# Kernel tuning notes

Measured on AMD Instinct MI355X. Metric: run time of the kernel, lower is better.

The kernel has to match this reference:

```python
import jax, jax.numpy as jnp
import numpy as np

FEAT_STRIDE = 16
PRE_NMS_TOP_N = 4000   # cfg[cfg_key].RPN_PRE_NMS_TOP_N
POST_NMS_TOP_N = 300   # cfg[cfg_key].RPN_POST_NMS_TOP_N
NMS_THRESH = 0.7       # cfg[cfg_key].RPN_NMS_THRESH


def _generate_anchors(base_size=16, ratios=(0.5, 1.0, 2.0), scales=(8, 16, 32)):
    ratios = np.array(ratios, dtype=np.float64)
    scales = np.array(scales, dtype=np.float64)
    base = np.array([1, 1, base_size, base_size], dtype=np.float64) - 1

    def whctrs(a):
        w = a[2] - a[0] + 1
        h = a[3] - a[1] + 1
        return w, h, a[0] + 0.5 * (w - 1), a[1] + 0.5 * (h - 1)

    def mk(ws, hs, xc, yc):
        ws = np.atleast_1d(ws)[:, None]
        hs = np.atleast_1d(hs)[:, None]
        return np.hstack((xc - 0.5 * (ws - 1), yc - 0.5 * (hs - 1),
                          xc + 0.5 * (ws - 1), yc + 0.5 * (hs - 1)))

    w, h, xc, yc = whctrs(base)
    size = w * h
    ws = np.round(np.sqrt(size / ratios))
    hs = np.round(ws * ratios)
    ratio_anchors = mk(ws, hs, xc, yc)
    out = []
    for i in range(ratio_anchors.shape[0]):
        w, h, xc, yc = whctrs(ratio_anchors[i])
        out.append(mk(w * scales, h * scales, xc, yc))
    return np.vstack(out).astype(np.float32)  # [9,4]


def _nms_keep(boxes, thresh):
    # boxes sorted by score desc, [N,4]; torchvision-style IoU (no +1).
    x1, y1, x2, y2 = boxes[:, 0], boxes[:, 1], boxes[:, 2], boxes[:, 3]
    areas = (x2 - x1) * (y2 - y1)
    lt = jnp.maximum(boxes[:, None, :2], boxes[None, :, :2])
    rb = jnp.minimum(boxes[:, None, 2:], boxes[None, :, 2:])
    wh = jnp.clip(rb - lt, 0.0)
    inter = wh[..., 0] * wh[..., 1]
    iou = inter / (areas[:, None] + areas[None, :] - inter + 1e-9)  # [N,N]
    N = boxes.shape[0]
    idx = jnp.arange(N)
    def body(i, keep):
        sup = (iou[i] > thresh) & (idx > i) & keep[i]
        return keep & ~sup
    return jax.lax.fori_loop(0, N, body, jnp.ones((N,), jnp.bool_))


def _per_image(boxes, scores):
    # pre-NMS top-k by score (matches sort-desc + slice)
    _, order = jax.lax.top_k(scores, PRE_NMS_TOP_N)
    b = boxes[order]
    keep = _nms_keep(jax.lax.stop_gradient(b), NMS_THRESH)
    rank = jnp.cumsum(keep) - 1                       # position among kept
    tgt = jnp.where(keep, rank, POST_NMS_TOP_N)       # OOB indices are dropped
    return jnp.zeros((POST_NMS_TOP_N, 4), boxes.dtype).at[tgt].set(b, mode='drop')


def reference(scores, bbox_deltas, im_info, anchors):
    B, A, H, W = scores.shape
    # anchor shifts over the feature grid
    sx = jnp.arange(W, dtype=scores.dtype) * FEAT_STRIDE
    sy = jnp.arange(H, dtype=scores.dtype) * FEAT_STRIDE
    yy, xx = jnp.meshgrid(sy, sx, indexing='ij')
    shifts = jnp.stack([xx.ravel(), yy.ravel(), xx.ravel(), yy.ravel()], axis=1)  # [K,4]
    all_anchors = (anchors[None, :, :] + shifts[:, None, :]).reshape(-1, 4)       # [K*A,4]

    deltas = bbox_deltas.transpose(0, 2, 3, 1).reshape(B, -1, 4)  # [B,K*A,4]
    sc = scores.transpose(0, 2, 3, 1).reshape(B, -1)              # [B,K*A]

    # bbox_transform_inv
    w = all_anchors[:, 2] - all_anchors[:, 0] + 1.0
    h = all_anchors[:, 3] - all_anchors[:, 1] + 1.0
    cx = all_anchors[:, 0] + 0.5 * w
    cy = all_anchors[:, 1] + 0.5 * h
    pcx = deltas[..., 0] * w + cx
    pcy = deltas[..., 1] * h + cy
    pw = jnp.exp(deltas[..., 2]) * w
    ph = jnp.exp(deltas[..., 3]) * h
    props = jnp.stack([pcx - 0.5 * pw, pcy - 0.5 * ph,
                       pcx + 0.5 * pw, pcy + 0.5 * ph], axis=-1)  # [B,K*A,4]

    # clip_boxes: x in [0, im_w-1], y in [0, im_h-1]
    hi = jnp.stack([im_info[:, 1] - 1, im_info[:, 0] - 1,
                    im_info[:, 1] - 1, im_info[:, 0] - 1], axis=1)  # [B,4]
    props = jnp.clip(props, 0.0, hi[:, None, :])

    boxes_out = jax.vmap(_per_image)(props, sc)  # [B,POST,4]
    batch_col = jnp.broadcast_to(
        jnp.arange(B, dtype=scores.dtype)[:, None, None], (B, POST_NMS_TOP_N, 1))
    return jnp.concatenate([batch_col, boxes_out], axis=-1)  # [B,POST,5]


def setup_inputs():
    key = jax.random.key(0)
    k1, k2 = jax.random.split(key)
    B, A, H, W = 4, 9, 50, 76
    scores = jax.random.normal(k1, (B, A, H, W), jnp.float32)
    bbox_deltas = jax.random.normal(k2, (B, 4 * A, H, W), jnp.float32) * 0.2
    im_info = jnp.tile(jnp.array([[800.0, 1216.0, 1.0]], jnp.float32), (B, 1))
    anchors = jnp.asarray(_generate_anchors())
    return {"scores": scores, "bbox_deltas": bbox_deltas,
            "im_info": im_info, "anchors": anchors}
```

## Files before the change

kernel.cpp:

```cpp
#include <hip/hip_runtime.h>
#include <stdint.h>

#define A_N 9
#define H_N 50
#define W_N 76
#define HW_N (H_N * W_N)
#define N_PROP (A_N * HW_N)
#define B_N 4
#define PRE_NMS 4000
#define POST_NMS 300
#define NMS_TH 0.7f
#define SORT_N 4096
#define MASK_WORDS 64
#define CAND_MAX 5120
#define NBINS 4096
#define NPAIR 32
#define NLW 5
#define NDELTA 6
#define DEC_BLKS ((N_PROP + 255) / 256)

__global__ __launch_bounds__(256) void decode_kernel(
    const float* __restrict__ scores,
    const float* __restrict__ deltas,
    const float* __restrict__ im_info,
    const float* __restrict__ anchors,
    float4* __restrict__ boxes,
    unsigned long long* __restrict__ keys) {
#pragma clang fp contract(off)
    int tid = threadIdx.x;
    int b = blockIdx.y;
    int r = blockIdx.x * 256 + tid;
    if (r >= N_PROP) return;

    int a = r / HW_N;
    int hw = r - a * HW_N;
    int hy = hw / W_N;
    int wx = hw - hy * W_N;

    float sx = (float)wx * 16.0f;
    float sy = (float)hy * 16.0f;
    float ax1 = anchors[a * 4 + 0] + sx;
    float ay1 = anchors[a * 4 + 1] + sy;
    float ax2 = anchors[a * 4 + 2] + sx;
    float ay2 = anchors[a * 4 + 3] + sy;
    float aw = ax2 - ax1 + 1.0f;
    float ah = ay2 - ay1 + 1.0f;
    float cx = ax1 + 0.5f * aw;
    float cy = ay1 + 0.5f * ah;

    const float* db = deltas + ((size_t)b * 36 + (size_t)a * 4) * HW_N + hw;
    float d0 = db[0];
    float d1 = db[HW_N];
    float d2 = db[2 * HW_N];
    float d3 = db[3 * HW_N];

    float pcx = d0 * aw + cx;
    float pcy = d1 * ah + cy;
    float pw  = expf(d2) * aw;
    float ph  = expf(d3) * ah;

    float x1 = pcx - 0.5f * pw;
    float y1 = pcy - 0.5f * ph;
    float x2 = pcx + 0.5f * pw;
    float y2 = pcy + 0.5f * ph;

    float xhi = im_info[b * 3 + 1] - 1.0f;
    float yhi = im_info[b * 3 + 0] - 1.0f;
    x1 = fminf(fmaxf(x1, 0.0f), xhi);
    y1 = fminf(fmaxf(y1, 0.0f), yhi);
    x2 = fminf(fmaxf(x2, 0.0f), xhi);
    y2 = fminf(fmaxf(y2, 0.0f), yhi);

    boxes[(size_t)b * N_PROP + r] = make_float4(x1, y1, x2, y2);

    float s = scores[((size_t)b * A_N + a) * HW_N + hw];
    unsigned f = __float_as_uint(s);
    unsigned sk = f ^ ((f & 0x80000000u) ? 0xFFFFFFFFu : 0x80000000u);
    unsigned n_ref = (unsigned)(hw * A_N + a);
    unsigned long long key = ((unsigned long long)sk << 32) | (unsigned)(~n_ref);
    keys[(size_t)b * N_PROP + r] = key;
}

__global__ __launch_bounds__(1024) void mid_kernel(
    const unsigned long long* __restrict__ keys,
    unsigned* __restrict__ cnt,
    unsigned long long* __restrict__ cand) {
    __shared__ unsigned hist[NBINS];
    __shared__ int Tlds;
    __shared__ unsigned cntL;
    const int b = blockIdx.x;
    const int tid = threadIdx.x;

    for (int i = tid; i < NBINS; i += 1024) hist[i] = 0u;
    if (tid == 0) cntL = 0u;
    __syncthreads();

    for (int it = 0; it < (N_PROP + 1023) / 1024; ++it) {
        int n = it * 1024 + tid;
        if (n < N_PROP) {
            unsigned long long k = keys[(size_t)b * N_PROP + n];
            atomicAdd(&hist[(unsigned)(k >> 52)], 1u);
        }
    }
    __syncthreads();

    if (tid < 64) {
        int lane = tid;
        unsigned gsum = 0;
        for (int j = 0; j < 64; ++j) gsum += hist[lane * 64 + j];
        unsigned s = gsum;
        for (int d = 1; d < 64; d <<= 1) {
            unsigned t = (unsigned)__shfl_down((int)s, d);
            if (lane + d < 64) s += t;
        }
        unsigned long long bal = __ballot(s >= PRE_NMS);
        int gstar = 63 - __builtin_clzll(bal);
        unsigned after = (gstar < 63)
            ? (unsigned)__builtin_amdgcn_readlane((int)s, gstar + 1) : 0u;
        unsigned R = PRE_NMS - after;
        unsigned s2 = hist[gstar * 64 + lane];
        for (int d = 1; d < 64; d <<= 1) {
            unsigned t = (unsigned)__shfl_down((int)s2, d);
            if (lane + d < 64) s2 += t;
        }
        unsigned long long bal2 = __ballot(s2 >= R);
        int j = 63 - __builtin_clzll(bal2);
        if (lane == 0) Tlds = gstar * 64 + j;
    }
    __syncthreads();

    const int Tb = Tlds;
    for (int it = 0; it < (N_PROP + 1023) / 1024; ++it) {
        int n = it * 1024 + tid;
        bool pred = false;
        unsigned long long k = 0ull;
        if (n < N_PROP) {
            k = keys[(size_t)b * N_PROP + n];
            pred = ((int)(unsigned)(k >> 52) >= Tb);
        }
        unsigned long long m = __ballot(pred);
        if (m) {
            int lane = tid & 63;
            int lead = __ffsll((unsigned long long)m) - 1;
            unsigned base = 0;
            if (lane == lead) base = atomicAdd(&cntL, (unsigned)__popcll(m));
            base = __shfl((int)base, lead);
            if (pred) {
                unsigned pos = base + (unsigned)__popcll(m & ((1ull << lane) - 1ull));
                if (pos < CAND_MAX) cand[(size_t)b * CAND_MAX + pos] = k;
            }
        }
    }
    __syncthreads();
    if (tid == 0) cnt[b] = cntL;
}

__global__ __launch_bounds__(256) void rank_scatter_kernel(
    const unsigned long long* __restrict__ cand,
    const unsigned* __restrict__ cnt,
    const float4* __restrict__ boxes,
    float4* __restrict__ sortedBoxes) {
    __shared__ unsigned long long sk[256];
    int b = blockIdx.y;
    int tid = threadIdx.x;
    int ci = blockIdx.x * 64 + (tid >> 2);
    int q = tid & 3;
    int mc = (int)min(cnt[b], (unsigned)CAND_MAX);
    unsigned long long my = (ci < mc) ? cand[(size_t)b * CAND_MAX + ci] : 0ull;
    int rank = 0;
    int nt = (mc + 255) >> 8;
    for (int t = 0; t < nt; ++t) {
        int j = t * 256 + tid;
        sk[tid] = (j < mc) ? cand[(size_t)b * CAND_MAX + j] : 0ull;
        __syncthreads();
#pragma unroll 16
        for (int c = 0; c < 64; ++c) {
            int cc = q * 64 + ((c + q * 17) & 63);
            rank += (sk[cc] > my) ? 1 : 0;
        }
        __syncthreads();
    }
    rank += __shfl_xor(rank, 1);
    rank += __shfl_xor(rank, 2);
    if (q == 0 && ci < mc && rank < PRE_NMS) {
        unsigned n_ref = ~(unsigned)(my & 0xFFFFFFFFull);
        unsigned a = n_ref % A_N;
        unsigned hw = n_ref / A_N;
        sortedBoxes[(size_t)b * SORT_N + rank] =
            boxes[(size_t)b * N_PROP + a * HW_N + hw];
    }
    if (q == 1) {
        int pi = blockIdx.x * 64 + (tid >> 2);
        if (pi >= PRE_NMS && pi < SORT_N)
            sortedBoxes[(size_t)b * SORT_N + pi] = make_float4(0.f, 0.f, 0.f, 0.f);
    }
}

__global__ __launch_bounds__(256) void iou_mask_kernel(
    const float4* __restrict__ sortedBoxes,
    unsigned long long* __restrict__ colmaj,
    unsigned long long* __restrict__ rowmaj,
    unsigned long long* __restrict__ trans) {
#pragma clang fp contract(off)
    int b = blockIdx.y;
    int wv = threadIdx.x >> 6;
    int t = threadIdx.x & 63;
    int k = blockIdx.x * 4 + wv;
    int rc = 0;
    while (k >= 64 - rc) { k -= 64 - rc; ++rc; }
    int cc = rc + k;

    __shared__ float4 colb[4][64];
    colb[wv][t] = sortedBoxes[(size_t)b * SORT_N + cc * 64 + t];
    __syncthreads();

    int r = rc * 64 + t;
    float4 rb = sortedBoxes[(size_t)b * SORT_N + r];
    float rarea = (rb.z - rb.x) * (rb.w - rb.y);
    unsigned long long word = 0ull;
    for (int c = 0; c < 64; ++c) {
        int j = cc * 64 + c;
        float4 cb = colb[wv][c];
        float carea = (cb.z - cb.x) * (cb.w - cb.y);
        float ltx = fmaxf(rb.x, cb.x);
        float lty = fmaxf(rb.y, cb.y);
        float rbx = fminf(rb.z, cb.z);
        float rby = fminf(rb.w, cb.w);
        float iw = fmaxf(rbx - ltx, 0.0f);
        float ih = fmaxf(rby - lty, 0.0f);
        float inter = iw * ih;
        float iou = inter / (rarea + carea - inter + 1e-9f);
        if (iou > NMS_TH && j > r) word |= (1ull << c);
    }
    colmaj[((size_t)b * MASK_WORDS + cc) * SORT_N + r] = word;
    rowmaj[((size_t)b * SORT_N + r) * MASK_WORDS + cc] = word;

    int delta = cc - rc;
    if (delta < NDELTA) {
        unsigned long long tw = 0ull;
        for (int j = 0; j < 64; ++j) {
            unsigned long long bal = __ballot(((word >> j) & 1ull) != 0ull);
            if (t == j) tw = bal;
        }
        trans[(((size_t)b * MASK_WORDS + rc) * NDELTA + delta) * 64 + t] = tw;
    }
}

__device__ __forceinline__ unsigned long long bal_nz(unsigned long long tileT,
                                                     unsigned long long alive) {
    return __ballot((tileT & alive) != 0ull);
}

__device__ __forceinline__ void block_sync() {
    asm volatile("s_waitcnt lgkmcnt(0)" ::: "memory");
    __builtin_amdgcn_s_barrier();
    asm volatile("" ::: "memory");
}

#define GLOAD(dst, addr) \
    asm volatile("global_load_dwordx2 %0, %1, off" : "=v"(dst) : "v"(addr))
#define WAITV0 asm volatile("s_waitcnt vmcnt(0)" ::: "memory")
#define SCHED0 __builtin_amdgcn_sched_barrier(0)

#define TRG(P, t)  ((t) < 6 ? 2 * (P) : 2 * (P) + 1)
#define TRD(P, t)  ((t) < 6 ? (t) : (t) - 6)
#define TRVAL(P, t) (TRG(P, t) + TRD(P, t) < 64)
#define TR_ADDR(P, t) \
    (TR + (((size_t)TRG(P, t) * NDELTA + (TRVAL(P, t) ? TRD(P, t) : 0)) << 6) + lane)

#define ISSUE_PAIR(P)                                                          \
    do {                                                                       \
        pf_vmask = 0u;                                                         \
        GLOAD(pf0,  TR_ADDR(P, 0));  if (TRVAL(P, 0))  pf_vmask |= 1u << 0;    \
        GLOAD(pf1,  TR_ADDR(P, 1));  if (TRVAL(P, 1))  pf_vmask |= 1u << 1;    \
        GLOAD(pf2,  TR_ADDR(P, 2));  if (TRVAL(P, 2))  pf_vmask |= 1u << 2;    \
        GLOAD(pf3,  TR_ADDR(P, 3));  if (TRVAL(P, 3))  pf_vmask |= 1u << 3;    \
        GLOAD(pf4,  TR_ADDR(P, 4));  if (TRVAL(P, 4))  pf_vmask |= 1u << 4;    \
        GLOAD(pf5,  TR_ADDR(P, 5));  if (TRVAL(P, 5))  pf_vmask |= 1u << 5;    \
        GLOAD(pf6,  TR_ADDR(P, 6));  if (TRVAL(P, 6))  pf_vmask |= 1u << 6;    \
        GLOAD(pf7,  TR_ADDR(P, 7));  if (TRVAL(P, 7))  pf_vmask |= 1u << 7;    \
        GLOAD(pf8,  TR_ADDR(P, 8));  if (TRVAL(P, 8))  pf_vmask |= 1u << 8;    \
        GLOAD(pf9,  TR_ADDR(P, 9));  if (TRVAL(P, 9))  pf_vmask |= 1u << 9;    \
        GLOAD(pf10, TR_ADDR(P, 10)); if (TRVAL(P, 10)) pf_vmask |= 1u << 10;   \
    } while (0)

#define NEXTROW2(rk)                                                           \
    int rk;                                                                    \
    {                                                                          \
        if (xA) { int bb_ = __builtin_ctzll(xA); xA &= xA - 1; rk = baseA + bb_; } \
        else if (xB) { int bb_ = __builtin_ctzll(xB); xB &= xB - 1; rk = baseB + bb_; } \
        else rk = rpad;                                                        \
    }

__global__ __launch_bounds__(512, 1) void nms_scan_kernel(
    const unsigned long long* __restrict__ trans,
    const unsigned long long* __restrict__ rowmaj,
    const float4* __restrict__ sortedBoxes,
    float* __restrict__ out) {
    int b = blockIdx.x;
    int tid = threadIdx.x;
    int lane = tid & 63;
    int wv = tid >> 6;
    const unsigned long long* TR = trans + (size_t)b * MASK_WORDS * NDELTA * 64;
    const unsigned long long* R = rowmaj + (size_t)b * SORT_N * MASK_WORDS;

    __shared__ int kept[POST_NMS];
    __shared__ unsigned remW[MASK_WORDS][2];
    __shared__ unsigned long long aliveLds[MASK_WORDS];
    __shared__ unsigned long long ring[4][11][64];
    __shared__ unsigned long long car2[2][2];
    __shared__ int doneLds;
    __shared__ int kcntLds;

    if (tid < MASK_WORDS) { remW[tid][0] = 0u; remW[tid][1] = 0u; aliveLds[tid] = 0ull; }
    if (tid < 4) car2[tid >> 1][tid & 1] = 0ull;
    if (tid == 0) { doneLds = 0; kcntLds = 0; }

    unsigned long long pf0=0,pf1=0,pf2=0,pf3=0,pf4=0,pf5=0,pf6=0,pf7=0,pf8=0,pf9=0,pf10=0;
    unsigned pf_vmask = 0u;
    bool pf_have = false;
    unsigned long long gp0=0,gp1=0,gp2=0,gp3=0,gp4=0,gp5=0,gp6=0,gp7=0;
    bool ld_valid = false;

    if (wv == 1) {
        for (int t = 0; t < 11; ++t) {
            unsigned long long v = TRVAL(0, t)
                ? TR[(((size_t)TRG(0, t)) * NDELTA + TRD(0, t)) * 64 + lane] : 0ull;
            ring[0][t][lane] = v;
        }
        ISSUE_PAIR(1);
        pf_have = true;
    }
    block_sync();

    unsigned long long carA = 0ull, carB = 0ull;
    int kcnt = 0;

    for (int q = 0; q < NPAIR; ++q) {
        if (wv == 0) {
            int A = 2 * q, Bg = A + 1, slot = q & 3;
            unsigned long long dA  = ring[slot][0][lane];
            unsigned long long tA1 = ring[slot][1][lane];
            unsigned long long tA2 = ring[slot][2][lane];
            unsigned long long tA3 = ring[slot][3][lane];
            unsigned long long dB  = ring[slot][6][lane];
            unsigned long long tB1 = ring[slot][7][lane];
            unsigned long long tB2 = ring[slot][8][lane];
            unsigned long long remA =
                ((unsigned long long)remW[A][1] << 32) | (unsigned long long)remW[A][0];
            unsigned long long remB =
                ((unsigned long long)remW[Bg][1] << 32) | (unsigned long long)remW[Bg][0];
            unsigned long long h2A = car2[q & 1][0];
            unsigned long long h2B = car2[q & 1][1];
            bool hit = false;
            unsigned long long aliveA = 0ull, aliveB = 0ull;
            unsigned long long pend = ~(remA | carA | h2A);
            while (pend) {
                int bit = __builtin_ctzll(pend);
                if (lane == 0) kept[kcnt] = (A << 6) + bit;
                ++kcnt;
                aliveA |= 1ull << bit;
                if (kcnt == POST_NMS) { hit = true; break; }
                unsigned long long d = __ballot(((dA >> bit) & 1ull) != 0ull);
                pend &= ~(d | (1ull << bit));
            }
            if (!hit) {
                unsigned long long nA1 = bal_nz(tA1, aliveA);
                pend = ~(remB | carB | h2B | nA1);
                while (pend) {
                    int bit = __builtin_ctzll(pend);
                    if (lane == 0) kept[kcnt] = (Bg << 6) + bit;
                    ++kcnt;
                    aliveB |= 1ull << bit;
                    if (kcnt == POST_NMS) { hit = true; break; }
                    unsigned long long d = __ballot(((dB >> bit) & 1ull) != 0ull);
                    pend &= ~(d | (1ull << bit));
                }
            }
            carA = bal_nz(tA2, aliveA) | bal_nz(tB1, aliveB);
            carB = bal_nz(tA3, aliveA) | bal_nz(tB2, aliveB);
            if (lane == 0) {
                aliveLds[A]  = aliveA;
                aliveLds[Bg] = aliveB;
                kcntLds = kcnt;
                if (hit) doneLds = 1;
            }
        } else if (wv == 1) {
            if (pf_have) {
                WAITV0;
                SCHED0;
                int wp = q + 1;
                if (wp < NPAIR) {
                    int ws = wp & 3;
                    ring[ws][0][lane]  = (pf_vmask & (1u << 0))  ? pf0  : 0ull;
                    ring[ws][1][lane]  = (pf_vmask & (1u << 1))  ? pf1  : 0ull;
                    ring[ws][2][lane]  = (pf_vmask & (1u << 2))  ? pf2  : 0ull;
                    ring[ws][3][lane]  = (pf_vmask & (1u << 3))  ? pf3  : 0ull;
                    ring[ws][4][lane]  = (pf_vmask & (1u << 4))  ? pf4  : 0ull;
                    ring[ws][5][lane]  = (pf_vmask & (1u << 5))  ? pf5  : 0ull;
                    ring[ws][6][lane]  = (pf_vmask & (1u << 6))  ? pf6  : 0ull;
                    ring[ws][7][lane]  = (pf_vmask & (1u << 7))  ? pf7  : 0ull;
                    ring[ws][8][lane]  = (pf_vmask & (1u << 8))  ? pf8  : 0ull;
                    ring[ws][9][lane]  = (pf_vmask & (1u << 9))  ? pf9  : 0ull;
                    ring[ws][10][lane] = (pf_vmask & (1u << 10)) ? pf10 : 0ull;
                }
                pf_have = false;
            }
            int ip = q + 2;
            if (ip < NPAIR) {
                ISSUE_PAIR(ip);
                pf_have = true;
            }
        } else if (wv == 2) {
            if (q >= 1) {
                int p = q - 1, sp = p & 3;
                unsigned long long aA = aliveLds[2 * p];
                unsigned long long aB = aliveLds[2 * p + 1];
                unsigned long long tA4 = ring[sp][4][lane];
                unsigned long long tA5 = ring[sp][5][lane];
                unsigned long long tB3 = ring[sp][9][lane];
                unsigned long long tB4 = ring[sp][10][lane];
                unsigned long long c0 = bal_nz(tA4, aA) | bal_nz(tB3, aB);
                unsigned long long c1 = bal_nz(tA5, aA) | bal_nz(tB4, aB);
                if (lane == 0) {
                    car2[(q + 1) & 1][0] = c0;
                    car2[(q + 1) & 1][1] = c1;
                }
            }
        } else {
            if (ld_valid) {
                WAITV0;
                SCHED0;
                unsigned long long acc =
                    ((gp0 | gp1) | (gp2 | gp3)) | ((gp4 | gp5) | (gp6 | gp7));
                unsigned lo = (unsigned)acc, hi = (unsigned)(acc >> 32);
                if (lo) atomicOr(&remW[lane][0], lo);
                if (hi) atomicOr(&remW[lane][1], hi);
                ld_valid = false;
            }
            if (q >= 1) {
                int p = q - 1, gA = 2 * p, gB = 2 * p + 1;
                unsigned long long aA = aliveLds[gA];
                unsigned long long aB = aliveLds[gB];
                int k = wv - 3;
                unsigned long long below = (1ull << lane) - 1ull;
                bool inA = (aA >> lane) & 1ull;
                bool inB = (aB >> lane) & 1ull;
                int posA = (int)__popcll(aA & below);
                int posB = (int)__popcll(aA) + (int)__popcll(aB & below);
                unsigned long long mA = __ballot(inA && (posA % NLW) == k);
                unsigned long long mB = __ballot(inB && (posB % NLW) == k);
                if (mA | mB) {
                    int baseA = gA << 6, baseB = gB << 6;
                    unsigned long long xA = mA, xB = mB;
                    int rpad = mA ? (baseA + __builtin_ctzll(mA))
                                  : (baseB + __builtin_ctzll(mB));
                    NEXTROW2(r0) NEXTROW2(r1) NEXTROW2(r2) NEXTROW2(r3)
                    NEXTROW2(r4) NEXTROW2(r5) NEXTROW2(r6) NEXTROW2(r7)
                    const unsigned long long* Rb = R + lane;
                    GLOAD(gp0, Rb + (size_t)r0 * MASK_WORDS);
                    GLOAD(gp1, Rb + (size_t)r1 * MASK_WORDS);
                    GLOAD(gp2, Rb + (size_t)r2 * MASK_WORDS);
                    GLOAD(gp3, Rb + (size_t)r3 * MASK_WORDS);
                    GLOAD(gp4, Rb + (size_t)r4 * MASK_WORDS);
                    GLOAD(gp5, Rb + (size_t)r5 * MASK_WORDS);
                    GLOAD(gp6, Rb + (size_t)r6 * MASK_WORDS);
                    GLOAD(gp7, Rb + (size_t)r7 * MASK_WORDS);
                    ld_valid = true;
                    unsigned long long ovf = 0ull;
                    while (xA) {
                        int bb = __builtin_ctzll(xA); xA &= xA - 1;
                        ovf |= Rb[(size_t)(baseA + bb) * MASK_WORDS];
                    }
                    while (xB) {
                        int bb = __builtin_ctzll(xB); xB &= xB - 1;
                        ovf |= Rb[(size_t)(baseB + bb) * MASK_WORDS];
                    }
                    if (ovf) {
                        unsigned lo = (unsigned)ovf, hi = (unsigned)(ovf >> 32);
                        if (lo) atomicOr(&remW[lane][0], lo);
                        if (hi) atomicOr(&remW[lane][1], hi);
                    }
                }
            }
        }
        block_sync();
        if (doneLds) break;
    }

    WAITV0;
    __syncthreads();

    int kc = kcntLds;
    for (int r = tid; r < POST_NMS; r += 512) {
        float* o = out + ((size_t)b * POST_NMS + r) * 5;
        float4 bx = make_float4(0.f, 0.f, 0.f, 0.f);
        if (r < kc) bx = sortedBoxes[(size_t)b * SORT_N + kept[r]];
        o[0] = (float)b;
        o[1] = bx.x;
        o[2] = bx.y;
        o[3] = bx.z;
        o[4] = bx.w;
    }
}

extern "C" void kernel_launch(void* const* d_in, const int* in_sizes, int n_in,
                              void* d_out, int out_size, void* d_ws, size_t ws_size,
                              hipStream_t stream) {
    const float* scores  = (const float*)d_in[0];
    const float* deltas  = (const float*)d_in[1];
    const float* im_info = (const float*)d_in[2];
    const float* anchors = (const float*)d_in[3];
    float* out = (float*)d_out;

    char* ws = (char*)d_ws;
    size_t off = 0;
    float4* boxes = (float4*)(ws + off);
    off += (size_t)B_N * N_PROP * sizeof(float4);
    off = (off + 255) & ~(size_t)255;
    unsigned long long* keys = (unsigned long long*)(ws + off);
    off += (size_t)B_N * N_PROP * sizeof(unsigned long long);
    off = (off + 255) & ~(size_t)255;
    float4* sortedBoxes = (float4*)(ws + off);
    off += (size_t)B_N * SORT_N * sizeof(float4);
    off = (off + 255) & ~(size_t)255;
    unsigned long long* colmaj = (unsigned long long*)(ws + off);
    off += (size_t)B_N * MASK_WORDS * SORT_N * sizeof(unsigned long long);
    off = (off + 255) & ~(size_t)255;
    unsigned long long* rowmaj = (unsigned long long*)(ws + off);
    off += (size_t)B_N * SORT_N * MASK_WORDS * sizeof(unsigned long long);
    off = (off + 255) & ~(size_t)255;
    unsigned long long* trans = (unsigned long long*)(ws + off);
    off += (size_t)B_N * MASK_WORDS * NDELTA * 64 * sizeof(unsigned long long);
    off = (off + 255) & ~(size_t)255;
    unsigned long long* cand = (unsigned long long*)(ws + off);
    off += (size_t)B_N * CAND_MAX * sizeof(unsigned long long);
    off = (off + 255) & ~(size_t)255;
    unsigned* cnt = (unsigned*)(ws + off);
    off += (size_t)B_N * sizeof(unsigned);

    decode_kernel<<<dim3(DEC_BLKS, B_N), 256, 0, stream>>>(
        scores, deltas, im_info, anchors, boxes, keys);
    mid_kernel<<<B_N, 1024, 0, stream>>>(keys, cnt, cand);
    rank_scatter_kernel<<<dim3(CAND_MAX / 64, B_N), 256, 0, stream>>>(
        cand, cnt, boxes, sortedBoxes);
    iou_mask_kernel<<<dim3(520, B_N), 256, 0, stream>>>(
        sortedBoxes, colmaj, rowmaj, trans);
    nms_scan_kernel<<<B_N, 512, 0, stream>>>(trans, rowmaj, sortedBoxes, out);
}
```

Before: 199.7 us.

## Fuse five kernels into two using global atomic gates between stages

Merges decode, histogram/threshold selection and rank-scatter into one kernel, and IoU mask and NMS scan into a second. Dependent blocks spin on device-scope atomic counters rather than waiting on kernel boundaries, which removes launch gaps between stages. The unused column-major mask write is dropped, and the IoU stage now uses 8 waves per block. Correctness relies on producer blocks being scheduled before or alongside the waiting consumers, so there is a deadlock risk if they are not. A memset of the gate counters is added to each call.

```diff
diff --git a/kernel.cpp b/kernel.cpp
--- a/kernel.cpp
+++ b/kernel.cpp
@@ -17,232 +17,204 @@
 #define NPAIR 32
 #define NLW 5
 #define NDELTA 6
-#define DEC_BLKS ((N_PROP + 255) / 256)
-
-__global__ __launch_bounds__(256) void decode_kernel(
+#define DEC_CHUNKS 134
+#define DEC_BLKS (DEC_CHUNKS * B_N)
+#define RANK_PB 80
+#define K1_BLKS (DEC_BLKS + B_N + RANK_PB * B_N)
+#define IOU_PB 260
+#define K2_BLKS (IOU_PB * B_N + B_N)
+
+__device__ __forceinline__ void gate_wait(unsigned* p, unsigned tgt) {
+    while (__hip_atomic_load(p, __ATOMIC_ACQUIRE, __HIP_MEMORY_SCOPE_AGENT) < tgt)
+        __builtin_amdgcn_s_sleep(8);
+}
+__device__ __forceinline__ void gate_signal(unsigned* p) {
+    __hip_atomic_fetch_add(p, 1u, __ATOMIC_RELEASE, __HIP_MEMORY_SCOPE_AGENT);
+}
+
+__global__ __launch_bounds__(256) void front_fused(
     const float* __restrict__ scores,
     const float* __restrict__ deltas,
     const float* __restrict__ im_info,
     const float* __restrict__ anchors,
     float4* __restrict__ boxes,
-    unsigned long long* __restrict__ keys) {
+    unsigned long long* __restrict__ keys,
+    unsigned* __restrict__ cnt,
+    unsigned long long* __restrict__ cand,
+    float4* __restrict__ sortedBoxes,
+    unsigned* __restrict__ dec_done,
+    unsigned* __restrict__ mid_done) {
 #pragma clang fp contract(off)
-    int tid = threadIdx.x;
-    int b = blockIdx.y;
-    int r = blockIdx.x * 256 + tid;
-    if (r >= N_PROP) return;
-
-    int a = r / HW_N;
-    int hw = r - a * HW_N;
-    int hy = hw / W_N;
-    int wx = hw - hy * W_N;
-
-    float sx = (float)wx * 16.0f;
-    float sy = (float)hy * 16.0f;
-    float ax1 = anchors[a * 4 + 0] + sx;
-    float ay1 = anchors[a * 4 + 1] + sy;
-    float ax2 = anchors[a * 4 + 2] + sx;
-    float ay2 = anchors[a * 4 + 3] + sy;
-    float aw = ax2 - ax1 + 1.0f;
-    float ah = ay2 - ay1 + 1.0f;
-    float cx = ax1 + 0.5f * aw;
-    float cy = ay1 + 0.5f * ah;
-
-    const float* db = deltas + ((size_t)b * 36 + (size_t)a * 4) * HW_N + hw;
-    float d0 = db[0];
-    float d1 = db[HW_N];
-    float d2 = db[2 * HW_N];
-    float d3 = db[3 * HW_N];
-
-    float pcx = d0 * aw + cx;
-    float pcy = d1 * ah + cy;
-    float pw  = expf(d2) * aw;
-    float ph  = expf(d3) * ah;
-
-    float x1 = pcx - 0.5f * pw;
-    float y1 = pcy - 0.5f * ph;
-    float x2 = pcx + 0.5f * pw;
-    float y2 = pcy + 0.5f * ph;
-
-    float xhi = im_info[b * 3 + 1] - 1.0f;
-    float yhi = im_info[b * 3 + 0] - 1.0f;
-    x1 = fminf(fmaxf(x1, 0.0f), xhi);
-    y1 = fminf(fmaxf(y1, 0.0f), yhi);
-    x2 = fminf(fmaxf(x2, 0.0f), xhi);
-    y2 = fminf(fmaxf(y2, 0.0f), yhi);
-
-    boxes[(size_t)b * N_PROP + r] = make_float4(x1, y1, x2, y2);
-
-    float s = scores[((size_t)b * A_N + a) * HW_N + hw];
-    unsigned f = __float_as_uint(s);
-    unsigned sk = f ^ ((f & 0x80000000u) ? 0xFFFFFFFFu : 0x80000000u);
-    unsigned n_ref = (unsigned)(hw * A_N + a);
-    unsigned long long key = ((unsigned long long)sk << 32) | (unsigned)(~n_ref);
-    keys[(size_t)b * N_PROP + r] = key;
-}
-
-__global__ __launch_bounds__(1024) void mid_kernel(
-    const unsigned long long* __restrict__ keys,
-    unsigned* __restrict__ cnt,
-    unsigned long long* __restrict__ cand) {
     __shared__ unsigned hist[NBINS];
+    __shared__ unsigned long long sk[256];
     __shared__ int Tlds;
     __shared__ unsigned cntL;
-    const int b = blockIdx.x;
     const int tid = threadIdx.x;
-
-    for (int i = tid; i < NBINS; i += 1024) hist[i] = 0u;
-    if (tid == 0) cntL = 0u;
-    __syncthreads();
-
-    for (int it = 0; it < (N_PROP + 1023) / 1024; ++it) {
-        int n = it * 1024 + tid;
-        if (n < N_PROP) {
-            unsigned long long k = keys[(size_t)b * N_PROP + n];
-            atomicAdd(&hist[(unsigned)(k >> 52)], 1u);
-        }
-    }
-    __syncthreads();
-
-    if (tid < 64) {
-        int lane = tid;
-        unsigned gsum = 0;
-        for (int j = 0; j < 64; ++j) gsum += hist[lane * 64 + j];
-        unsigned s = gsum;
-        for (int d = 1; d < 64; d <<= 1) {
-            unsigned t = (unsigned)__shfl_down((int)s, d);
-            if (lane + d < 64) s += t;
-        }
-        unsigned long long bal = __ballot(s >= PRE_NMS);
-        int gstar = 63 - __builtin_clzll(bal);
-        unsigned after = (gstar < 63)
-            ? (unsigned)__builtin_amdgcn_readlane((int)s, gstar + 1) : 0u;
-        unsigned R = PRE_NMS - after;
-        unsigned s2 = hist[gstar * 64 + lane];
-        for (int d = 1; d < 64; d <<= 1) {
-            unsigned t = (unsigned)__shfl_down((int)s2, d);
-            if (lane + d < 64) s2 += t;
-        }
-        unsigned long long bal2 = __ballot(s2 >= R);
-        int j = 63 - __builtin_clzll(bal2);
-        if (lane == 0) Tlds = gstar * 64 + j;
-    }
-    __syncthreads();
-
-    const int Tb = Tlds;
-    for (int it = 0; it < (N_PROP + 1023) / 1024; ++it) {
-        int n = it * 1024 + tid;
-        bool pred = false;
-        unsigned long long k = 0ull;
-        if (n < N_PROP) {
-            k = keys[(size_t)b * N_PROP + n];
-            pred = ((int)(unsigned)(k >> 52) >= Tb);
-        }
-        unsigned long long m = __ballot(pred);
-        if (m) {
-            int lane = tid & 63;
-            int lead = __ffsll((unsigned long long)m) - 1;
-            unsigned base = 0;
-            if (lane == lead) base = atomicAdd(&cntL, (unsigned)__popcll(m));
-            base = __shfl((int)base, lead);
-            if (pred) {
-                unsigned pos = base + (unsigned)__popcll(m & ((1ull << lane) - 1ull));
-                if (pos < CAND_MAX) cand[(size_t)b * CAND_MAX + pos] = k;
-            }
-        }
-    }
-    __syncthreads();
-    if (tid == 0) cnt[b] = cntL;
-}
-
-__global__ __launch_bounds__(256) void rank_scatter_kernel(
-    const unsigned long long* __restrict__ cand,
-    const unsigned* __restrict__ cnt,
-    const float4* __restrict__ boxes,
-    float4* __restrict__ sortedBoxes) {
-    __shared__ unsigned long long sk[256];
-    int b = blockIdx.y;
-    int tid = threadIdx.x;
-    int ci = blockIdx.x * 64 + (tid >> 2);
-    int q = tid & 3;
-    int mc = (int)min(cnt[b], (unsigned)CAND_MAX);
-    unsigned long long my = (ci < mc) ? cand[(size_t)b * CAND_MAX + ci] : 0ull;
-    int rank = 0;
-    int nt = (mc + 255) >> 8;
-    for (int t = 0; t < nt; ++t) {
-        int j = t * 256 + tid;
-        sk[tid] = (j < mc) ? cand[(size_t)b * CAND_MAX + j] : 0ull;
-        __syncthreads();
+    const int bid = blockIdx.x;
+
+    if (bid < DEC_BLKS) {
+        int b = bid & 3;
+        int r = (bid >> 2) * 256 + tid;
+        if (r < N_PROP) {
+            int a = r / HW_N;
+            int hw = r - a * HW_N;
+            int hy = hw / W_N;
+            int wx = hw - hy * W_N;
+
+            float sx = (float)wx * 16.0f;
+            float sy = (float)hy * 16.0f;
+            float ax1 = anchors[a * 4 + 0] + sx;
+            float ay1 = anchors[a * 4 + 1] + sy;
+            float ax2 = anchors[a * 4 + 2] + sx;
+            float ay2 = anchors[a * 4 + 3] + sy;
+            float aw = ax2 - ax1 + 1.0f;
+            float ah = ay2 - ay1 + 1.0f;
+            float cx = ax1 + 0.5f * aw;
+            float cy = ay1 + 0.5f * ah;
+
+            const float* db = deltas + ((size_t)b * 36 + (size_t)a * 4) * HW_N + hw;
+            float d0 = db[0];
+            float d1 = db[HW_N];
+            float d2 = db[2 * HW_N];
+            float d3 = db[3 * HW_N];
+
+            float pcx = d0 * aw + cx;
+            float pcy = d1 * ah + cy;
+            float pw  = expf(d2) * aw;
+            float ph  = expf(d3) * ah;
+
+            float x1 = pcx - 0.5f * pw;
+            float y1 = pcy - 0.5f * ph;
+            float x2 = pcx + 0.5f * pw;
+            float y2 = pcy + 0.5f * ph;
+
+            float xhi = im_info[b * 3 + 1] - 1.0f;
+            float yhi = im_info[b * 3 + 0] - 1.0f;
+            x1 = fminf(fmaxf(x1, 0.0f), xhi);
+            y1 = fminf(fmaxf(y1, 0.0f), yhi);
+            x2 = fminf(fmaxf(x2, 0.0f), xhi);
+            y2 = fminf(fmaxf(y2, 0.0f), yhi);
+
+            boxes[(size_t)b * N_PROP + r] = make_float4(x1, y1, x2, y2);
+
+            float s = scores[((size_t)b * A_N + a) * HW_N + hw];
+            unsigned f = __float_as_uint(s);
+            unsigned skk = f ^ ((f & 0x80000000u) ? 0xFFFFFFFFu : 0x80000000u);
+            unsigned n_ref = (unsigned)(hw * A_N + a);
+            unsigned long long key =
+                ((unsigned long long)skk << 32) | (unsigned)(~n_ref);
+            keys[(size_t)b * N_PROP + r] = key;
+        }
+        __syncthreads();
+        if (tid == 0) gate_signal(&dec_done[b]);
+    } else if (bid < DEC_BLKS + B_N) {
+        int b = bid - DEC_BLKS;
+        for (int i = tid; i < NBINS; i += 256) hist[i] = 0u;
+        if (tid == 0) {
+            cntL = 0u;
+            gate_wait(&dec_done[b], DEC_CHUNKS);
+        }
+        __syncthreads();
+
+        for (int it = 0; it < DEC_CHUNKS; ++it) {
+            int n = it * 256 + tid;
+            if (n < N_PROP) {
+                unsigned long long k = keys[(size_t)b * N_PROP + n];
+                atomicAdd(&hist[(unsigned)(k >> 52)], 1u);
+            }
+        }
+        __syncthreads();
+
+        if (tid < 64) {
+            int lane = tid;
+            unsigned gsum = 0;
+            for (int j = 0; j < 64; ++j) gsum += hist[lane * 64 + j];
+            unsigned s = gsum;
+            for (int d = 1; d < 64; d <<= 1) {
+                unsigned t = (unsigned)__shfl_down((int)s, d);
+                if (lane + d < 64) s += t;
+            }
+            unsigned long long bal = __ballot(s >= PRE_NMS);
+            int gstar = 63 - __builtin_clzll(bal);
+            unsigned after = (gstar < 63)
+                ? (unsigned)__builtin_amdgcn_readlane((int)s, gstar + 1) : 0u;
+            unsigned R = PRE_NMS - after;
+            unsigned s2 = hist[gstar * 64 + lane];
+            for (int d = 1; d < 64; d <<= 1) {
+                unsigned t = (unsigned)__shfl_down((int)s2, d);
+                if (lane + d < 64) s2 += t;
+            }
+            unsigned long long bal2 = __ballot(s2 >= R);
+            int j = 63 - __builtin_clzll(bal2);
+            if (lane == 0) Tlds = gstar * 64 + j;
+        }
+        __syncthreads();
+
+        const int Tb = Tlds;
+        for (int it = 0; it < DEC_CHUNKS; ++it) {
+            int n = it * 256 + tid;
+            bool pred = false;
+            unsigned long long k = 0ull;
+            if (n < N_PROP) {
+                k = keys[(size_t)b * N_PROP + n];
+                pred = ((int)(unsigned)(k >> 52) >= Tb);
+            }
+            unsigned long long m = __ballot(pred);
+            if (m) {
+                int lane = tid & 63;
+                int lead = __ffsll((unsigned long long)m) - 1;
+                unsigned base = 0;
+                if (lane == lead) base = atomicAdd(&cntL, (unsigned)__popcll(m));
+                base = __shfl((int)base, lead);
+                if (pred) {
+                    unsigned pos = base + (unsigned)__popcll(m & ((1ull << lane) - 1ull));
+                    if (pos < CAND_MAX) cand[(size_t)b * CAND_MAX + pos] = k;
+                }
+            }
+        }
+        __syncthreads();
+        if (tid == 0) {
+            cnt[b] = cntL;
+            gate_signal(&mid_done[b]);
+        }
+    } else {
+        int i = bid - (DEC_BLKS + B_N);
+        int b = i / RANK_PB;
+        int cblk = i - b * RANK_PB;
+        if (tid == 0) gate_wait(&mid_done[b], 1u);
+        __syncthreads();
+
+        int ci = cblk * 64 + (tid >> 2);
+        int q = tid & 3;
+        int mc = (int)min(cnt[b], (unsigned)CAND_MAX);
+        unsigned long long my = (ci < mc) ? cand[(size_t)b * CAND_MAX + ci] : 0ull;
+        int rank = 0;
+        int nt = (mc + 255) >> 8;
+        for (int t = 0; t < nt; ++t) {
+            int j = t * 256 + tid;
+            sk[tid] = (j < mc) ? cand[(size_t)b * CAND_MAX + j] : 0ull;
+            __syncthreads();
 #pragma unroll 16
-        for (int c = 0; c < 64; ++c) {
-            int cc = q * 64 + ((c + q * 17) & 63);
-            rank += (sk[cc] > my) ? 1 : 0;
-        }
-        __syncthreads();
-    }
-    rank += __shfl_xor(rank, 1);
-    rank += __shfl_xor(rank, 2);
-    if (q == 0 && ci < mc && rank < PRE_NMS) {
-        unsigned n_ref = ~(unsigned)(my & 0xFFFFFFFFull);
-        unsigned a = n_ref % A_N;
-        unsigned hw = n_ref / A_N;
-        sortedBoxes[(size_t)b * SORT_N + rank] =
-            boxes[(size_t)b * N_PROP + a * HW_N + hw];
-    }
-    if (q == 1) {
-        int pi = blockIdx.x * 64 + (tid >> 2);
-        if (pi >= PRE_NMS && pi < SORT_N)
-            sortedBoxes[(size_t)b * SORT_N + pi] = make_float4(0.f, 0.f, 0.f, 0.f);
-    }
-}
-
-__global__ __launch_bounds__(256) void iou_mask_kernel(
-    const float4* __restrict__ sortedBoxes,
-    unsigned long long* __restrict__ colmaj,
-    unsigned long long* __restrict__ rowmaj,
-    unsigned long long* __restrict__ trans) {
-#pragma clang fp contract(off)
-    int b = blockIdx.y;
-    int wv = threadIdx.x >> 6;
-    int t = threadIdx.x & 63;
-    int k = blockIdx.x * 4 + wv;
-    int rc = 0;
-    while (k >= 64 - rc) { k -= 64 - rc; ++rc; }
-    int cc = rc + k;
-
-    __shared__ float4 colb[4][64];
-    colb[wv][t] = sortedBoxes[(size_t)b * SORT_N + cc * 64 + t];
-    __syncthreads();
-
-    int r = rc * 64 + t;
-    float4 rb = sortedBoxes[(size_t)b * SORT_N + r];
-    float rarea = (rb.z - rb.x) * (rb.w - rb.y);
-    unsigned long long word = 0ull;
-    for (int c = 0; c < 64; ++c) {
-        int j = cc * 64 + c;
-        float4 cb = colb[wv][c];
-        float carea = (cb.z - cb.x) * (cb.w - cb.y);
-        float ltx = fmaxf(rb.x, cb.x);
-        float lty = fmaxf(rb.y, cb.y);
-        float rbx = fminf(rb.z, cb.z);
-        float rby = fminf(rb.w, cb.w);
-        float iw = fmaxf(rbx - ltx, 0.0f);
-        float ih = fmaxf(rby - lty, 0.0f);
-        float inter = iw * ih;
-        float iou = inter / (rarea + carea - inter + 1e-9f);
-        if (iou > NMS_TH && j > r) word |= (1ull << c);
-    }
-    colmaj[((size_t)b * MASK_WORDS + cc) * SORT_N + r] = word;
-    rowmaj[((size_t)b * SORT_N + r) * MASK_WORDS + cc] = word;
-
-    int delta = cc - rc;
-    if (delta < NDELTA) {
-        unsigned long long tw = 0ull;
-        for (int j = 0; j < 64; ++j) {
-            unsigned long long bal = __ballot(((word >> j) & 1ull) != 0ull);
-            if (t == j) tw = bal;
-        }
-        trans[(((size_t)b * MASK_WORDS + rc) * NDELTA + delta) * 64 + t] = tw;
+            for (int c = 0; c < 64; ++c) {
+                int cc = q * 64 + ((c + q * 17) & 63);
+                rank += (sk[cc] > my) ? 1 : 0;
+            }
+            __syncthreads();
+        }
+        rank += __shfl_xor(rank, 1);
+        rank += __shfl_xor(rank, 2);
+        if (q == 0 && ci < mc && rank < PRE_NMS) {
+            unsigned n_ref = ~(unsigned)(my & 0xFFFFFFFFull);
+            unsigned a = n_ref % A_N;
+            unsigned hw = n_ref / A_N;
+            sortedBoxes[(size_t)b * SORT_N + rank] =
+                boxes[(size_t)b * N_PROP + a * HW_N + hw];
+        }
+        if (q == 1) {
+            int pi = cblk * 64 + (tid >> 2);
+            if (pi >= PRE_NMS && pi < SORT_N)
+                sortedBoxes[(size_t)b * SORT_N + pi] = make_float4(0.f, 0.f, 0.f, 0.f);
+        }
     }
 }
 
@@ -292,18 +264,64 @@
         else rk = rpad;                                                        \
     }
 
-__global__ __launch_bounds__(512, 1) void nms_scan_kernel(
-    const unsigned long long* __restrict__ trans,
-    const unsigned long long* __restrict__ rowmaj,
+__global__ __launch_bounds__(512, 1) void back_fused(
     const float4* __restrict__ sortedBoxes,
+    unsigned long long* __restrict__ rowmaj,
+    unsigned long long* __restrict__ trans,
+    unsigned* __restrict__ iou_done,
     float* __restrict__ out) {
-    int b = blockIdx.x;
-    int tid = threadIdx.x;
-    int lane = tid & 63;
-    int wv = tid >> 6;
-    const unsigned long long* TR = trans + (size_t)b * MASK_WORDS * NDELTA * 64;
-    const unsigned long long* R = rowmaj + (size_t)b * SORT_N * MASK_WORDS;
-
+#pragma clang fp contract(off)
+    const int tid = threadIdx.x;
+    const int bid = blockIdx.x;
+    const int lane = tid & 63;
+    const int wv = tid >> 6;
+
+    if (bid < IOU_PB * B_N) {
+        int b = bid / IOU_PB;
+        int k = (bid - b * IOU_PB) * 8 + wv;
+        int rc = 0;
+        while (k >= 64 - rc) { k -= 64 - rc; ++rc; }
+        int cc = rc + k;
+
+        __shared__ float4 colb[8][64];
+        colb[wv][lane] = sortedBoxes[(size_t)b * SORT_N + cc * 64 + lane];
+        __syncthreads();
+
+        int r = rc * 64 + lane;
+        float4 rb = sortedBoxes[(size_t)b * SORT_N + r];
+        float rarea = (rb.z - rb.x) * (rb.w - rb.y);
+        unsigned long long word = 0ull;
+        for (int c = 0; c < 64; ++c) {
+            int j = cc * 64 + c;
+            float4 cb = colb[wv][c];
+            float carea = (cb.z - cb.x) * (cb.w - cb.y);
+            float ltx = fmaxf(rb.x, cb.x);
+            float lty = fmaxf(rb.y, cb.y);
+            float rbx = fminf(rb.z, cb.z);
+            float rby = fminf(rb.w, cb.w);
+            float iw = fmaxf(rbx - ltx, 0.0f);
+            float ih = fmaxf(rby - lty, 0.0f);
+            float inter = iw * ih;
+            float iou = inter / (rarea + carea - inter + 1e-9f);
+            if (iou > NMS_TH && j > r) word |= (1ull << c);
+        }
+        rowmaj[((size_t)b * SORT_N + r) * MASK_WORDS + cc] = word;
+
+        int delta = cc - rc;
+        if (delta < NDELTA) {
+            unsigned long long tw = 0ull;
+            for (int j = 0; j < 64; ++j) {
+                unsigned long long bal = __ballot(((word >> j) & 1ull) != 0ull);
+                if (lane == j) tw = bal;
+            }
+            trans[(((size_t)b * MASK_WORDS + rc) * NDELTA + delta) * 64 + lane] = tw;
+        }
+        __syncthreads();
+        if (tid == 0) gate_signal(&iou_done[b]);
+        return;
+    }
+
+    int b = bid - IOU_PB * B_N;
     __shared__ int kept[POST_NMS];
     __shared__ unsigned remW[MASK_WORDS][2];
     __shared__ unsigned long long aliveLds[MASK_WORDS];
@@ -314,7 +332,14 @@
 
     if (tid < MASK_WORDS) { remW[tid][0] = 0u; remW[tid][1] = 0u; aliveLds[tid] = 0ull; }
     if (tid < 4) car2[tid >> 1][tid & 1] = 0ull;
-    if (tid == 0) { doneLds = 0; kcntLds = 0; }
+    if (tid == 0) {
+        doneLds = 0; kcntLds = 0;
+        gate_wait(&iou_done[b], IOU_PB);
+    }
+    __syncthreads();
+
+    const unsigned long long* TR = trans + (size_t)b * MASK_WORDS * NDELTA * 64;
+    const unsigned long long* R = rowmaj + (size_t)b * SORT_N * MASK_WORDS;
 
     unsigned long long pf0=0,pf1=0,pf2=0,pf3=0,pf4=0,pf5=0,pf6=0,pf7=0,pf8=0,pf9=0,pf10=0;
     unsigned pf_vmask = 0u;
@@ -524,9 +549,6 @@
     float4* sortedBoxes = (float4*)(ws + off);
     off += (size_t)B_N * SORT_N * sizeof(float4);
     off = (off + 255) & ~(size_t)255;
-    unsigned long long* colmaj = (unsigned long long*)(ws + off);
-    off += (size_t)B_N * MASK_WORDS * SORT_N * sizeof(unsigned long long);
-    off = (off + 255) & ~(size_t)255;
     unsigned long long* rowmaj = (unsigned long long*)(ws + off);
     off += (size_t)B_N * SORT_N * MASK_WORDS * sizeof(unsigned long long);
     off = (off + 255) & ~(size_t)255;
@@ -538,13 +560,16 @@
     off = (off + 255) & ~(size_t)255;
     unsigned* cnt = (unsigned*)(ws + off);
     off += (size_t)B_N * sizeof(unsigned);
-
-    decode_kernel<<<dim3(DEC_BLKS, B_N), 256, 0, stream>>>(
-        scores, deltas, im_info, anchors, boxes, keys);
-    mid_kernel<<<B_N, 1024, 0, stream>>>(keys, cnt, cand);
-    rank_scatter_kernel<<<dim3(CAND_MAX / 64, B_N), 256, 0, stream>>>(
-        cand, cnt, boxes, sortedBoxes);
-    iou_mask_kernel<<<dim3(520, B_N), 256, 0, stream>>>(
-        sortedBoxes, colmaj, rowmaj, trans);
-    nms_scan_kernel<<<B_N, 512, 0, stream>>>(trans, rowmaj, sortedBoxes, out);
-}
+    off = (off + 255) & ~(size_t)255;
+    unsigned* gates = (unsigned*)(ws + off);
+    size_t gate_bytes = 12 * sizeof(unsigned);
+    off += gate_bytes;
+
+    hipMemsetAsync((void*)gates, 0, gate_bytes, stream);
+
+    front_fused<<<K1_BLKS, 256, 0, stream>>>(
+        scores, deltas, im_info, anchors, boxes, keys, cnt, cand, sortedBoxes,
+        gates + 0, gates + 4);
+    back_fused<<<K2_BLKS, 512, 0, stream>>>(
+        sortedBoxes, rowmaj, trans, gates + 8, out);
+}
```

Result: slower. 668.6 us (+234.8%).
